# Optimization experiments

Hardware: AMD Instinct MI355X
Metric: run time of the kernel (lower is better)

The kernel has to match this reference:

```python
import jax, jax.numpy as jnp
import numpy as np

B, S, D_MODEL = 2, 2048, 2048
NUM_HEADS, NUM_KV_HEADS, HEAD_DIM = 16, 4, 128
MAX_SEQ = 2048
ROPE_WAVELENGTH = 10000.0


def apply_rope(x, positions, head_dim, max_wavelength):
    # x: [B, S, H, D], positions: [B, S]
    fraction = 2.0 * jnp.arange(0, head_dim // 2, dtype=jnp.float32) / head_dim
    timescale = max_wavelength ** fraction                      # [D/2]
    sinusoid = positions[..., None].astype(jnp.float32) / timescale  # [B,S,D/2]
    sin = jnp.sin(sinusoid)[:, :, None, :]                      # [B,S,1,D/2]
    cos = jnp.cos(sinusoid)[:, :, None, :]
    x1, x2 = jnp.split(x, 2, axis=-1)
    first = x1 * cos - x2 * sin
    second = x2 * cos + x1 * sin
    return jnp.concatenate([first, second], axis=-1).astype(x.dtype)


def setup_inputs() -> dict:
    key = jax.random.key(0)
    ks = jax.random.split(key, 5)
    inputs = jax.random.normal(ks[0], (B, S, D_MODEL), dtype=jnp.float32)
    seq_pos = jnp.broadcast_to(jnp.arange(S, dtype=jnp.int32)[None, :], (B, S))
    std = 0.01  # nnx.initializers.normal() default stddev
    wq = jax.random.normal(ks[1], (D_MODEL, NUM_HEADS, HEAD_DIM), dtype=jnp.float32) * std
    bq = jnp.zeros((NUM_HEADS, HEAD_DIM), dtype=jnp.float32)
    wkv = jax.random.normal(ks[2], (D_MODEL, NUM_KV_HEADS, 2 * HEAD_DIM), dtype=jnp.float32) * std
    bkv = jnp.zeros((NUM_KV_HEADS, 2 * HEAD_DIM), dtype=jnp.float32)
    wo = jax.random.normal(ks[3], (NUM_HEADS, HEAD_DIM, D_MODEL), dtype=jnp.float32) * std
    bo = jnp.zeros((D_MODEL,), dtype=jnp.float32)
    return {"inputs": inputs, "seq_pos": seq_pos, "wq": wq, "bq": bq,
            "wkv": wkv, "bkv": bkv, "wo": wo, "bo": bo}


def reference(inputs, seq_pos, wq, bq, wkv, bkv, wo, bo):
    dtype = inputs.dtype
    # Projections
    kv = jnp.einsum('bsd,dkh->bskh', inputs, wkv) + bkv          # [B,S,KV,2*HD]
    key, value = jnp.split(kv, 2, axis=-1)                       # [B,S,KV,HD] each
    query = jnp.einsum('bsd,dnh->bsnh', inputs, wq) + bq         # [B,S,H,HD]
    # RoPE
    query = apply_rope(query, seq_pos, HEAD_DIM, ROPE_WAVELENGTH)
    key = apply_rope(key, seq_pos, HEAD_DIM, ROPE_WAVELENGTH)
    # GQA: repeat KV heads
    rep = NUM_HEADS // NUM_KV_HEADS
    key_r = jnp.repeat(key, rep, axis=2)                          # [B,S,H,HD]
    value_r = jnp.repeat(value, rep, axis=2)
    # Attention (einsum_attention path)
    q = query / jnp.sqrt(jnp.asarray(HEAD_DIM, dtype=dtype))
    attn = jnp.einsum('bqhd,bkhd->bhqk', q, key_r)               # [B,H,S,S]
    # position_mask: seq_range <= time_steps -> causal
    seq_range = jnp.arange(MAX_SEQ, dtype=jnp.int32)
    mask = (seq_range[None, None, :] <= seq_pos[:, :, None])[:, None, :, :]  # [B,1,S,S]
    big_neg = jnp.finfo(dtype).min
    attn = jnp.where(mask, attn, big_neg)
    attn = jax.nn.softmax(attn, axis=-1).astype(dtype)
    x = jnp.einsum('bhqk,bkhd->bqhd', attn, value_r)             # [B,S,H,HD]
    out = jnp.einsum('bqhd,hdo->bqo', x, wo) + bo                # [B,S,D]
    return out
```

## Files before the change

### kernel.cpp

```cpp
#include <hip/hip_runtime.h>
#include <hip/hip_bf16.h>

#define DM    2048
#define SEQ   2048
#define NB    2
#define NH    16
#define NKVH  4
#define HD    128
#define NQKV  3072
#define MROWS 4096
#define KVB   64

using f32x4  = __attribute__((ext_vector_type(4))) float;
using short8 = __attribute__((ext_vector_type(8))) short;
using ushort8 = __attribute__((ext_vector_type(8))) unsigned short;

static __device__ __forceinline__ unsigned short f2bf(float f) {
  __hip_bfloat16 h = __float2bfloat16(f);
  return *reinterpret_cast<unsigned short*>(&h);
}
static __device__ __forceinline__ float bf2f(unsigned short u) {
  union { unsigned int i; float f; } v; v.i = ((unsigned int)u) << 16; return v.f;
}

typedef __attribute__((address_space(1))) const unsigned char as1_c;
typedef __attribute__((address_space(3))) unsigned char as3_c;
static __device__ __forceinline__ void gload_lds16(const void* g, void* l) {
  __builtin_amdgcn_global_load_lds((as1_c*)g, (as3_c*)l, 16, 0, 0);
}


__global__ void build_trig(float2* __restrict__ tbl) {
  int i = blockIdx.x * 256 + threadIdx.x;
  int p = i >> 6, d = i & 63;
  float inv_ts = powf(10000.0f, -(float)d * (1.0f / 64.0f));
  float ang = (float)p * inv_ts;
  float sn, cs;
  sincosf(ang, &sn, &cs);
  tbl[i] = make_float2(cs, sn);
}


__global__ void f32_to_bf16_vec(const float* __restrict__ src, unsigned short* __restrict__ dst, int n4) {
  int i = blockIdx.x * blockDim.x + threadIdx.x;
  if (i < n4) {
    float4 v = reinterpret_cast<const float4*>(src)[i];
    ushort4 o;
    o.x = f2bf(v.x); o.y = f2bf(v.y); o.z = f2bf(v.z); o.w = f2bf(v.w);
    reinterpret_cast<ushort4*>(dst)[i] = o;
  }
}

__global__ void transpose_all(const float* __restrict__ wq, const float* __restrict__ wkv,
                              const float* __restrict__ wo,
                              unsigned short* __restrict__ WqkvT, unsigned short* __restrict__ WoT) {
  int bx = blockIdx.x;
  const float* src; unsigned short* dst; int N;
  if (bx < 64)       { src = wq;  dst = WqkvT;                         N = 2048; }
  else if (bx < 96)  { src = wkv; dst = WqkvT + (size_t)2048 * DM;     N = 1024; bx -= 64; }
  else               { src = wo;  dst = WoT;                           N = 2048; bx -= 96; }
  __shared__ float t[32][33];
  int n0 = bx * 32, k0 = blockIdx.y * 32;
  int tx = threadIdx.x, ty = threadIdx.y;
  for (int j = 0; j < 4; j++)
    t[ty + j * 8][tx] = src[(size_t)(k0 + ty + j * 8) * N + n0 + tx];
  __syncthreads();
  for (int j = 0; j < 4; j++)
    dst[(size_t)(n0 + ty + j * 8) * DM + k0 + tx] = f2bf(t[tx][ty + j * 8]);
}

__global__ void bias_concat(const float* __restrict__ bq, const float* __restrict__ bkv, float* __restrict__ o) {
  int i = blockIdx.x * 256 + threadIdx.x;
  if (i < NQKV) o[i] = (i < DM) ? bq[i] : bkv[i - DM];
}


__global__ __launch_bounds__(256) void gemm_qkv(const unsigned short* __restrict__ A,
                                                const unsigned short* __restrict__ Bt,
                                                const float* __restrict__ bias,
                                                const int* __restrict__ seq_pos,
                                                const float2* __restrict__ tbl,
                                                unsigned short* __restrict__ Qo,
                                                unsigned short* __restrict__ Ko,
                                                unsigned short* __restrict__ Vo) {
  __shared__ __align__(16) unsigned short smem[128 * 136];
  unsigned short* la = smem;
  unsigned short* lb = smem + 128 * 64;
  const int K = DM;
  int tid = threadIdx.x, lane = tid & 63, w = tid >> 6;
  int wr = w >> 1, wc = w & 1, lg = lane >> 4, ln = lane & 15;
  int m0 = blockIdx.y * 128, n0 = blockIdx.x * 128;

  f32x4 acc[4][4];
  for (int mi = 0; mi < 4; mi++)
    for (int ni = 0; ni < 4; ni++) acc[mi][ni] = (f32x4){0, 0, 0, 0};

  int srow = lane >> 3;
  int scol = (lane & 7) * 8;
  const unsigned short* ga = A + (size_t)(m0 + w * 32 + srow) * K + scol;
  const unsigned short* gb = Bt + (size_t)(n0 + w * 32 + srow) * K + scol;
  unsigned short* lab = &la[(w * 32) * 64];
  unsigned short* lbb = &lb[(w * 32) * 64];

  for (int kt = 0; kt < K; kt += 64) {
#pragma unroll
    for (int i = 0; i < 4; i++) {
      gload_lds16(ga + (size_t)i * 8 * K + kt, lab + i * 8 * 64);
      gload_lds16(gb + (size_t)i * 8 * K + kt, lbb + i * 8 * 64);
    }
    __syncthreads();
#pragma unroll
    for (int kk = 0; kk < 64; kk += 32) {
      short8 af[4], bfr[4];
#pragma unroll
      for (int mi = 0; mi < 4; mi++)
        af[mi] = *reinterpret_cast<const short8*>(&la[(wr * 64 + mi * 16 + ln) * 64 + kk + lg * 8]);
#pragma unroll
      for (int ni = 0; ni < 4; ni++)
        bfr[ni] = *reinterpret_cast<const short8*>(&lb[(wc * 64 + ni * 16 + ln) * 64 + kk + lg * 8]);
#pragma unroll
      for (int mi = 0; mi < 4; mi++)
#pragma unroll
        for (int ni = 0; ni < 4; ni++)
          acc[mi][ni] = __builtin_amdgcn_mfma_f32_16x16x32_bf16(af[mi], bfr[ni], acc[mi][ni], 0, 0, 0);
    }
    __syncthreads();
  }

  __syncthreads();
#pragma unroll
  for (int mi = 0; mi < 4; mi++) {
    int row = wr * 64 + mi * 16 + lg * 4;
#pragma unroll
    for (int ni = 0; ni < 4; ni++) {
      int col = wc * 64 + ni * 16 + ln;
      float bv = bias[n0 + col];
#pragma unroll
      for (int r4 = 0; r4 < 4; r4++)
        smem[(row + r4) * 136 + col] = f2bf(acc[mi][ni][r4] + bv);
    }
  }
  __syncthreads();

  int nt = blockIdx.x;
  int b = m0 >> 11, s0 = m0 & (SEQ - 1);

  if (nt < 16 || !((nt - 16) & 1)) {
    float scale; unsigned short* dst;
    if (nt < 16) { scale = 0.08838834764831845f; dst = Qo + ((size_t)(b * NH + nt) * SEQ) * HD; }
    else         { scale = 1.0f; dst = Ko + ((size_t)(b * NKVH + ((nt - 16) >> 1)) * SEQ) * HD; }
    int sl = tid >> 1, dh = (tid & 1) * 32;
    int sg = s0 + sl;
    int pos = seq_pos[b * SEQ + sg];
    const float2* tp = tbl + pos * 64 + dh;
    ushort8 fb[4], sb2[4];
#pragma unroll
    for (int j = 0; j < 32; j++) {
      float x1 = bf2f(smem[sl * 136 + dh + j]);
      float x2 = bf2f(smem[sl * 136 + dh + j + 64]);
      float2 cs = tp[j];
      fb[j >> 3][j & 7]  = f2bf((x1 * cs.x - x2 * cs.y) * scale);
      sb2[j >> 3][j & 7] = f2bf((x2 * cs.x + x1 * cs.y) * scale);
    }
    unsigned short* dp = dst + (size_t)sg * HD + dh;
#pragma unroll
    for (int k = 0; k < 4; k++) {
      *reinterpret_cast<ushort8*>(dp + k * 8)      = fb[k];
      *reinterpret_cast<ushort8*>(dp + 64 + k * 8) = sb2[k];
    }
  } else {
    int kvh = (nt - 16) >> 1;
    int d = tid >> 1, sh = (tid & 1) * 64;
    ushort8 vb[8];
#pragma unroll
    for (int j = 0; j < 64; j++)
      vb[j >> 3][j & 7] = smem[(sh + j) * 136 + d];
    unsigned short* dp = Vo + ((size_t)(b * NKVH + kvh) * HD + d) * SEQ + s0 + sh;
#pragma unroll
    for (int k = 0; k < 8; k++)
      *reinterpret_cast<ushort8*>(dp + k * 8) = vb[k];
  }
}


__global__ __launch_bounds__(256) void gemm_bt(const unsigned short* __restrict__ A,
                                               const unsigned short* __restrict__ Bt,
                                               const float* __restrict__ bias,
                                               float* __restrict__ C, int M, int N, int K) {
  __shared__ __align__(16) unsigned short la[128 * 64];
  __shared__ __align__(16) unsigned short lb[128 * 64];
  int tid = threadIdx.x, lane = tid & 63, w = tid >> 6;
  int wr = w >> 1, wc = w & 1, lg = lane >> 4, ln = lane & 15;
  int m0 = blockIdx.y * 128, n0 = blockIdx.x * 128;

  f32x4 acc[4][4];
  for (int mi = 0; mi < 4; mi++)
    for (int ni = 0; ni < 4; ni++) acc[mi][ni] = (f32x4){0, 0, 0, 0};

  int srow = lane >> 3, scol = (lane & 7) * 8;
  const unsigned short* ga = A + (size_t)(m0 + w * 32 + srow) * K + scol;
  const unsigned short* gb = Bt + (size_t)(n0 + w * 32 + srow) * K + scol;
  unsigned short* lab = &la[(w * 32) * 64];
  unsigned short* lbb = &lb[(w * 32) * 64];

  for (int kt = 0; kt < K; kt += 64) {
#pragma unroll
    for (int i = 0; i < 4; i++) {
      gload_lds16(ga + (size_t)i * 8 * K + kt, lab + i * 8 * 64);
      gload_lds16(gb + (size_t)i * 8 * K + kt, lbb + i * 8 * 64);
    }
    __syncthreads();
#pragma unroll
    for (int kk = 0; kk < 64; kk += 32) {
      short8 af[4], bfr[4];
#pragma unroll
      for (int mi = 0; mi < 4; mi++)
        af[mi] = *reinterpret_cast<const short8*>(&la[(wr * 64 + mi * 16 + ln) * 64 + kk + lg * 8]);
#pragma unroll
      for (int ni = 0; ni < 4; ni++)
        bfr[ni] = *reinterpret_cast<const short8*>(&lb[(wc * 64 + ni * 16 + ln) * 64 + kk + lg * 8]);
#pragma unroll
      for (int mi = 0; mi < 4; mi++)
#pragma unroll
        for (int ni = 0; ni < 4; ni++)
          acc[mi][ni] = __builtin_amdgcn_mfma_f32_16x16x32_bf16(af[mi], bfr[ni], acc[mi][ni], 0, 0, 0);
    }
    __syncthreads();
  }
  for (int mi = 0; mi < 4; mi++) {
    int mrow = m0 + wr * 64 + mi * 16 + lg * 4;
    for (int ni = 0; ni < 4; ni++) {
      int n = n0 + wc * 64 + ni * 16 + ln;
      float bv = bias[n];
      for (int r4 = 0; r4 < 4; r4++)
        C[(size_t)(mrow + r4) * N + n] = acc[mi][ni][r4] + bv;
    }
  }
}


__global__ __launch_bounds__(256) void flash_attn(const unsigned short* __restrict__ Q,
                                                  const unsigned short* __restrict__ Kr,
                                                  const unsigned short* __restrict__ Vt,
                                                  const int* __restrict__ seq_pos,
                                                  unsigned short* __restrict__ X) {
  __shared__ __align__(16) unsigned short lds_k[64 * 128];
  __shared__ __align__(16) unsigned short lds_v[128 * 64];
  __shared__ __align__(16) unsigned short lds_p[4][16 * 64];
  int tid = threadIdx.x, lane = tid & 63, w = tid >> 6;
  int bh = blockIdx.y, b = bh >> 4, h = bh & 15, kvh = h >> 2;
  int lg = lane >> 4, ln = lane & 15;

  const unsigned short* kbase = Kr + ((size_t)(b * NKVH + kvh)) * SEQ * HD;
  const unsigned short* vbase = Vt + ((size_t)(b * NKVH + kvh)) * HD * SEQ;

  const unsigned short* gks[4]; unsigned short* lks[4];
  const unsigned short* gvs[4]; unsigned short* lvs[4];
#pragma unroll
  for (int i = 0; i < 4; i++) {
    int kr = w * 16 + i * 4 + (lane >> 4);
    int kc = (lane & 15) ^ (kr & 7);
    gks[i] = kbase + (size_t)kr * HD + kc * 8;
    lks[i] = lds_k + (w * 16 + i * 4) * 128;
    int vr = w * 32 + i * 8 + (lane >> 3);
    int vc = (lane & 7) ^ (vr & 7);
    gvs[i] = vbase + (size_t)vr * SEQ + vc * 8;
    lvs[i] = lds_v + (w * 32 + i * 8) * 64;
  }

  const short8 ones = {0x3F80, 0x3F80, 0x3F80, 0x3F80, 0x3F80, 0x3F80, 0x3F80, 0x3F80};

  for (int pass = 0; pass < 2; pass++) {
    int qtile = (pass == 0) ? (int)blockIdx.x : (SEQ / 64 - 1 - (int)blockIdx.x);
    int qblk = qtile * 64;
    int q0w = qblk + w * 16;

    int pmax = seq_pos[b * SEQ + qblk + lane];
    for (int o = 32; o; o >>= 1) { int t2 = __shfl_xor(pmax, o); pmax = pmax > t2 ? pmax : t2; }
    int ntiles = (pmax + KVB) >> 6;
    if (ntiles > SEQ / KVB) ntiles = SEQ / KVB;

    int pos_r[4];
    for (int r = 0; r < 4; r++) pos_r[r] = seq_pos[b * SEQ + q0w + lg * 4 + r];

    short8 qf[4];
    {
      const unsigned short* qp = Q + ((size_t)((b * NH + h) * SEQ + q0w + ln)) * HD;
      for (int c = 0; c < 4; c++) qf[c] = *reinterpret_cast<const short8*>(qp + c * 32 + lg * 8);
    }

    f32x4 acc[8];
    for (int dt = 0; dt < 8; dt++) acc[dt] = (f32x4){0, 0, 0, 0};
    f32x4 lacc = (f32x4){0, 0, 0, 0};
    float m_r[4] = {-1e30f, -1e30f, -1e30f, -1e30f};

    for (int t = 0; t < ntiles; t++) {
      int kv0 = t * KVB;
#pragma unroll
      for (int i = 0; i < 4; i++) {
        gload_lds16(gks[i] + (size_t)kv0 * HD, lks[i]);
        gload_lds16(gvs[i] + kv0, lvs[i]);
      }
      __syncthreads();

      f32x4 sa[4];
#pragma unroll
      for (int ct = 0; ct < 4; ct++) {
        sa[ct] = (f32x4){0, 0, 0, 0};
        int row = ct * 16 + ln;
        const char* kr0 = (const char*)lds_k + row * 256;
        int sw = (row & 7) << 4;
#pragma unroll
        for (int c = 0; c < 4; c++) {
          short8 kf = *reinterpret_cast<const short8*>(kr0 + ((c * 64 + lg * 16) ^ sw));
          sa[ct] = __builtin_amdgcn_mfma_f32_16x16x32_bf16(qf[c], kf, sa[ct], 0, 0, 0);
        }
      }

      float p[4][4], corr[4];
#pragma unroll
      for (int r = 0; r < 4; r++) {
        int kv = kv0 + ln;
        float v0 = (kv      <= pos_r[r]) ? sa[0][r] : -1e30f;
        float v1 = (kv + 16 <= pos_r[r]) ? sa[1][r] : -1e30f;
        float v2 = (kv + 32 <= pos_r[r]) ? sa[2][r] : -1e30f;
        float v3 = (kv + 48 <= pos_r[r]) ? sa[3][r] : -1e30f;
        float tmx = fmaxf(fmaxf(v0, v1), fmaxf(v2, v3));
        tmx = fmaxf(tmx, __shfl_xor(tmx, 1));
        tmx = fmaxf(tmx, __shfl_xor(tmx, 2));
        tmx = fmaxf(tmx, __shfl_xor(tmx, 4));
        tmx = fmaxf(tmx, __shfl_xor(tmx, 8));
        float nm = fmaxf(m_r[r], tmx);
        corr[r] = __expf(m_r[r] - nm);
        p[0][r] = __expf(v0 - nm); p[1][r] = __expf(v1 - nm);
        p[2][r] = __expf(v2 - nm); p[3][r] = __expf(v3 - nm);
        m_r[r] = nm;
      }

      {
        char* pw = (char*)lds_p[w];
#pragma unroll
        for (int r = 0; r < 4; r++) {
          int row = lg * 4 + r;
          int sw2 = (row & 7) << 4;
          char* pr = pw + row * 128;
#pragma unroll
          for (int ct = 0; ct < 4; ct++)
            *reinterpret_cast<unsigned short*>(pr + (((ct * 16 + ln) * 2) ^ sw2)) = f2bf(p[ct][r]);
        }
      }

#pragma unroll
      for (int dt = 0; dt < 8; dt++)
#pragma unroll
        for (int r = 0; r < 4; r++) acc[dt][r] *= corr[r];
#pragma unroll
      for (int r = 0; r < 4; r++) lacc[r] *= corr[r];

      asm volatile("s_waitcnt lgkmcnt(0)" ::: "memory");
      __builtin_amdgcn_sched_barrier(0);
      short8 pf[2];
      {
        const char* pr = (const char*)lds_p[w] + ln * 128;
        int sw2 = (ln & 7) << 4;
        pf[0] = *reinterpret_cast<const short8*>(pr + ((lg * 16) ^ sw2));
        pf[1] = *reinterpret_cast<const short8*>(pr + ((64 + lg * 16) ^ sw2));
      }

#pragma unroll
      for (int dt = 0; dt < 8; dt++) {
        int row = dt * 16 + ln;
        const char* vr0 = (const char*)lds_v + row * 128;
        int sw3 = (row & 7) << 4;
        short8 vf0 = *reinterpret_cast<const short8*>(vr0 + ((lg * 16) ^ sw3));
        short8 vf1 = *reinterpret_cast<const short8*>(vr0 + ((64 + lg * 16) ^ sw3));
        acc[dt] = __builtin_amdgcn_mfma_f32_16x16x32_bf16(pf[0], vf0, acc[dt], 0, 0, 0);
        acc[dt] = __builtin_amdgcn_mfma_f32_16x16x32_bf16(pf[1], vf1, acc[dt], 0, 0, 0);
      }
      lacc = __builtin_amdgcn_mfma_f32_16x16x32_bf16(pf[0], ones, lacc, 0, 0, 0);
      lacc = __builtin_amdgcn_mfma_f32_16x16x32_bf16(pf[1], ones, lacc, 0, 0, 0);
      __syncthreads();
    }

    for (int r = 0; r < 4; r++) {
      float inv = lacc[r] > 0.0f ? 1.0f / lacc[r] : 0.0f;
      int qrow = q0w + lg * 4 + r;
      unsigned short* xp = X + ((size_t)(b * SEQ + qrow)) * DM + h * HD;
      for (int dt = 0; dt < 8; dt++) xp[dt * 16 + ln] = f2bf(acc[dt][r] * inv);
    }
  }
}


extern "C" void kernel_launch(void* const* d_in, const int* in_sizes, int n_in,
                              void* d_out, int out_size, void* d_ws, size_t ws_size,
                              hipStream_t stream) {
  const float* inputs  = (const float*)d_in[0];
  const int*   seq_pos = (const int*)d_in[1];
  const float* wq  = (const float*)d_in[2];
  const float* bq  = (const float*)d_in[3];
  const float* wkv = (const float*)d_in[4];
  const float* bkv = (const float*)d_in[5];
  const float* wo  = (const float*)d_in[6];
  const float* bo  = (const float*)d_in[7];
  float* out = (float*)d_out;

  char* ws = (char*)d_ws;
  unsigned short* Abf     = (unsigned short*)(ws + 0);
  unsigned short* WqkvT   = (unsigned short*)(ws + 16777216);
  unsigned short* WoT     = (unsigned short*)(ws + 29360128);
  float*          biasqkv = (float*)(ws + 37748736);
  float2*         tbl     = (float2*)(ws + 37761024);
  unsigned short* Qr      = (unsigned short*)(ws + 38809600);
  unsigned short* Kr      = (unsigned short*)(ws + 55586816);
  unsigned short* Vt      = (unsigned short*)(ws + 59781120);
  unsigned short* Xb      = (unsigned short*)(ws + 63975424);

  build_trig<<<512, 256, 0, stream>>>(tbl);
  f32_to_bf16_vec<<<8192, 256, 0, stream>>>(inputs, Abf, (NB * SEQ * DM) / 4);
  transpose_all<<<dim3(160, 64), dim3(32, 8), 0, stream>>>(wq, wkv, wo, WqkvT, WoT);
  bias_concat<<<12, 256, 0, stream>>>(bq, bkv, biasqkv);

  gemm_qkv<<<dim3(NQKV / 128, MROWS / 128), 256, 0, stream>>>(
      Abf, WqkvT, biasqkv, seq_pos, tbl, Qr, Kr, Vt);

  flash_attn<<<dim3(SEQ / 128, NB * NH), 256, 0, stream>>>(Qr, Kr, Vt, seq_pos, Xb);

  gemm_bt<<<dim3(DM / 128, MROWS / 128), 256, 0, stream>>>(
      Xb, WoT, bo, out, MROWS, DM, DM);
}
```

Baseline: 362.3 us.

## Replace both projection GEMMs with pipelined 256x256 8-wave templated GEMM

Replaces the 128x128 single-buffered QKV and output GEMMs with one templated 256x256-tile, 512-thread kernel. It double-buffers LDS with interleaved async global-to-LDS loads between MFMA quarters and XOR-swizzles LDS to avoid bank conflicts. It also adds block-index swizzling for L2 locality and setprio around MFMA bursts. The QKV epilogue now applies RoPE, scaling and the V transpose straight from registers rather than through LDS. This trades a larger tile, more registers and a fixed 2-block occupancy for higher MFMA utilization and fewer blocks, which leaves fewer tiles per CU (192/128 blocks).

Result: faster. 314.6 us (-13.2%).

```diff
diff --git a/kernel.cpp b/kernel.cpp
--- a/kernel.cpp
+++ b/kernel.cpp
@@ -10,6 +10,7 @@
 #define NQKV  3072
 #define MROWS 4096
 #define KVB   64
+#define QSC   0.08838834764831845f
 
 using f32x4  = __attribute__((ext_vector_type(4))) float;
 using short8 = __attribute__((ext_vector_type(8))) short;
@@ -75,165 +76,176 @@
 }
 
 
-__global__ __launch_bounds__(256) void gemm_qkv(const unsigned short* __restrict__ A,
-                                                const unsigned short* __restrict__ Bt,
-                                                const float* __restrict__ bias,
-                                                const int* __restrict__ seq_pos,
-                                                const float2* __restrict__ tbl,
-                                                unsigned short* __restrict__ Qo,
-                                                unsigned short* __restrict__ Ko,
-                                                unsigned short* __restrict__ Vo) {
-  __shared__ __align__(16) unsigned short smem[128 * 136];
-  unsigned short* la = smem;
-  unsigned short* lb = smem + 128 * 64;
-  const int K = DM;
+#define STA(buf, kt, q) gload_lds16(gA + (size_t)((q) * 32) * K + (kt), LW + (buf) * 65536 + ((q) * 32 + rowA) * 128)
+#define STB(buf, kt, h) gload_lds16(gB + (size_t)((h) * 64) * K + (kt), LW + (buf) * 65536 + 32768 + ((h) * 64 + rowB) * 128)
+
+#define RDB(buf) \
+  _Pragma("unroll") for (int ni = 0; ni < 4; ++ni) { \
+    int row_ = (EPI == 1) ? (wc * 16 + ni * 64 + ln) : (wc * 64 + ni * 16 + ln); \
+    const char* p_ = (const char*)LW + (buf) * 65536 + 32768 + row_ * 128; \
+    bfr[ni][0] = *(const short8*)(p_ + coff0); \
+    bfr[ni][1] = *(const short8*)(p_ + coff1); }
+
+#define RDA(buf, q) \
+  _Pragma("unroll") for (int m2 = 0; m2 < 2; ++m2) { \
+    int row_ = wr * 128 + ((q) * 2 + m2) * 16 + ln; \
+    const char* p_ = (const char*)LW + (buf) * 65536 + row_ * 128; \
+    af[m2][0] = *(const short8*)(p_ + coff0); \
+    af[m2][1] = *(const short8*)(p_ + coff1); }
+
+#define MFQ(q) \
+  _Pragma("unroll") for (int m2 = 0; m2 < 2; ++m2) \
+  _Pragma("unroll") for (int ni = 0; ni < 4; ++ni) { \
+    acc[(q) * 2 + m2][ni] = __builtin_amdgcn_mfma_f32_16x16x32_bf16(af[m2][0], bfr[ni][0], acc[(q) * 2 + m2][ni], 0, 0, 0); \
+    acc[(q) * 2 + m2][ni] = __builtin_amdgcn_mfma_f32_16x16x32_bf16(af[m2][1], bfr[ni][1], acc[(q) * 2 + m2][ni], 0, 0, 0); }
+
+#define SYNC_IN() do { __builtin_amdgcn_sched_barrier(0); __builtin_amdgcn_s_barrier(); \
+  asm volatile("s_waitcnt lgkmcnt(0)" ::: "memory"); __builtin_amdgcn_sched_barrier(0); \
+  __builtin_amdgcn_s_setprio(1); } while (0)
+#define SYNC_OUT() do { __builtin_amdgcn_s_setprio(0); __builtin_amdgcn_sched_barrier(0); \
+  __builtin_amdgcn_s_barrier(); } while (0)
+#define SYNC_OUT_VM() do { __builtin_amdgcn_s_setprio(0); \
+  asm volatile("s_waitcnt vmcnt(6)" ::: "memory"); __builtin_amdgcn_sched_barrier(0); \
+  __builtin_amdgcn_s_barrier(); } while (0)
+
+template <int EPI>
+__global__ __launch_bounds__(512, 2) void gemm8(
+    const unsigned short* __restrict__ A, const unsigned short* __restrict__ Bt,
+    const float* __restrict__ bias, const int* __restrict__ seq_pos,
+    const float2* __restrict__ tbl,
+    unsigned short* __restrict__ Qo, unsigned short* __restrict__ Ko,
+    unsigned short* __restrict__ Vo, float* __restrict__ Cout,
+    int nbx, int N, int K) {
+  __shared__ __align__(16) unsigned short lds[2 * 2 * 16384];
   int tid = threadIdx.x, lane = tid & 63, w = tid >> 6;
-  int wr = w >> 1, wc = w & 1, lg = lane >> 4, ln = lane & 15;
-  int m0 = blockIdx.y * 128, n0 = blockIdx.x * 128;
-
-  f32x4 acc[4][4];
-  for (int mi = 0; mi < 4; mi++)
-    for (int ni = 0; ni < 4; ni++) acc[mi][ni] = (f32x4){0, 0, 0, 0};
-
-  int srow = lane >> 3;
-  int scol = (lane & 7) * 8;
-  const unsigned short* ga = A + (size_t)(m0 + w * 32 + srow) * K + scol;
-  const unsigned short* gb = Bt + (size_t)(n0 + w * 32 + srow) * K + scol;
-  unsigned short* lab = &la[(w * 32) * 64];
-  unsigned short* lbb = &lb[(w * 32) * 64];
-
-  for (int kt = 0; kt < K; kt += 64) {
-#pragma unroll
-    for (int i = 0; i < 4; i++) {
-      gload_lds16(ga + (size_t)i * 8 * K + kt, lab + i * 8 * 64);
-      gload_lds16(gb + (size_t)i * 8 * K + kt, lbb + i * 8 * 64);
-    }
-    __syncthreads();
-#pragma unroll
-    for (int kk = 0; kk < 64; kk += 32) {
-      short8 af[4], bfr[4];
-#pragma unroll
-      for (int mi = 0; mi < 4; mi++)
-        af[mi] = *reinterpret_cast<const short8*>(&la[(wr * 64 + mi * 16 + ln) * 64 + kk + lg * 8]);
-#pragma unroll
-      for (int ni = 0; ni < 4; ni++)
-        bfr[ni] = *reinterpret_cast<const short8*>(&lb[(wc * 64 + ni * 16 + ln) * 64 + kk + lg * 8]);
-#pragma unroll
-      for (int mi = 0; mi < 4; mi++)
-#pragma unroll
-        for (int ni = 0; ni < 4; ni++)
-          acc[mi][ni] = __builtin_amdgcn_mfma_f32_16x16x32_bf16(af[mi], bfr[ni], acc[mi][ni], 0, 0, 0);
-    }
-    __syncthreads();
+  int wr = w >> 2, wc = w & 3;
+  int lg = lane >> 4, ln = lane & 15;
+
+  int bid = blockIdx.x;
+  int cpx = gridDim.x >> 3;
+  int swz = (bid & 7) * cpx + (bid >> 3);
+  int by = swz / nbx, bx = swz - by * nbx;
+  int m0 = by * 256, n0 = bx * 256;
+
+  int soff = ((lane & 7) ^ (lane >> 3)) << 3;
+  const unsigned short* gA = A + (size_t)(m0 + ((w & 3) << 3) + ((w >> 2) << 7) + (lane >> 3)) * K + soff;
+  const unsigned short* gB = Bt + (size_t)(n0 + (w << 3) + (lane >> 3)) * K + soff;
+  char* LW = (char*)lds;
+  int rowA = ((w & 3) << 3) + ((w >> 2) << 7);
+  int rowB = (w << 3);
+  int coff0 = ((lg)     ^ (ln & 7)) << 4;
+  int coff1 = ((lg + 4) ^ (ln & 7)) << 4;
+
+  f32x4 acc[8][4];
+#pragma unroll
+  for (int mi = 0; mi < 8; ++mi)
+#pragma unroll
+    for (int ni = 0; ni < 4; ++ni) acc[mi][ni] = (f32x4){0, 0, 0, 0};
+
+  short8 bfr[4][2], af[2][2];
+
+  STB(0, 0, 0); STB(0, 0, 1); STB(0, 0, 2); STB(0, 0, 3);
+  STA(0, 0, 0); STA(0, 0, 1); STA(0, 0, 2); STA(0, 0, 3);
+  STB(1, 64, 0); STB(1, 64, 1); STB(1, 64, 2); STB(1, 64, 3);
+  STA(1, 64, 0); STA(1, 64, 1);
+  asm volatile("s_waitcnt vmcnt(6)" ::: "memory");
+  __builtin_amdgcn_sched_barrier(0);
+  __builtin_amdgcn_s_barrier();
+
+  for (int it = 0; it < (K >> 7); ++it) {
+    int kt1  = it * 128 + 64;
+    int ktn0 = (it * 128 + 128) & (K - 1);
+    int ktn1 = (it * 128 + 192) & (K - 1);
+    RDB(0); RDA(0, 0);
+    STA(1, kt1, 2); STA(1, kt1, 3);
+    SYNC_IN(); MFQ(0); SYNC_OUT();
+    RDA(0, 1);
+    STB(0, ktn0, 0); STB(0, ktn0, 1);
+    SYNC_IN(); MFQ(1); SYNC_OUT();
+    RDA(0, 2);
+    STB(0, ktn0, 2); STB(0, ktn0, 3);
+    SYNC_IN(); MFQ(2); SYNC_OUT();
+    RDA(0, 3);
+    STA(0, ktn0, 0); STA(0, ktn0, 1);
+    SYNC_IN(); MFQ(3); SYNC_OUT_VM();
+    RDB(1); RDA(1, 0);
+    STA(0, ktn0, 2); STA(0, ktn0, 3);
+    SYNC_IN(); MFQ(0); SYNC_OUT();
+    RDA(1, 1);
+    STB(1, ktn1, 0); STB(1, ktn1, 1);
+    SYNC_IN(); MFQ(1); SYNC_OUT();
+    RDA(1, 2);
+    STB(1, ktn1, 2); STB(1, ktn1, 3);
+    SYNC_IN(); MFQ(2); SYNC_OUT();
+    RDA(1, 3);
+    STA(1, ktn1, 0); STA(1, ktn1, 1);
+    SYNC_IN(); MFQ(3); SYNC_OUT_VM();
   }
-
-  __syncthreads();
-#pragma unroll
-  for (int mi = 0; mi < 4; mi++) {
-    int row = wr * 64 + mi * 16 + lg * 4;
-#pragma unroll
-    for (int ni = 0; ni < 4; ni++) {
-      int col = wc * 64 + ni * 16 + ln;
-      float bv = bias[n0 + col];
-#pragma unroll
-      for (int r4 = 0; r4 < 4; r4++)
-        smem[(row + r4) * 136 + col] = f2bf(acc[mi][ni][r4] + bv);
-    }
-  }
-  __syncthreads();
-
-  int nt = blockIdx.x;
-  int b = m0 >> 11, s0 = m0 & (SEQ - 1);
-
-  if (nt < 16 || !((nt - 16) & 1)) {
-    float scale; unsigned short* dst;
-    if (nt < 16) { scale = 0.08838834764831845f; dst = Qo + ((size_t)(b * NH + nt) * SEQ) * HD; }
-    else         { scale = 1.0f; dst = Ko + ((size_t)(b * NKVH + ((nt - 16) >> 1)) * SEQ) * HD; }
-    int sl = tid >> 1, dh = (tid & 1) * 32;
-    int sg = s0 + sl;
-    int pos = seq_pos[b * SEQ + sg];
-    const float2* tp = tbl + pos * 64 + dh;
-    ushort8 fb[4], sb2[4];
-#pragma unroll
-    for (int j = 0; j < 32; j++) {
-      float x1 = bf2f(smem[sl * 136 + dh + j]);
-      float x2 = bf2f(smem[sl * 136 + dh + j + 64]);
-      float2 cs = tp[j];
-      fb[j >> 3][j & 7]  = f2bf((x1 * cs.x - x2 * cs.y) * scale);
-      sb2[j >> 3][j & 7] = f2bf((x2 * cs.x + x1 * cs.y) * scale);
-    }
-    unsigned short* dp = dst + (size_t)sg * HD + dh;
-#pragma unroll
-    for (int k = 0; k < 4; k++) {
-      *reinterpret_cast<ushort8*>(dp + k * 8)      = fb[k];
-      *reinterpret_cast<ushort8*>(dp + 64 + k * 8) = sb2[k];
+  asm volatile("s_waitcnt vmcnt(0)" ::: "memory");
+
+  if constexpr (EPI == 0) {
+#pragma unroll
+    for (int mi = 0; mi < 8; ++mi) {
+      int row = m0 + wr * 128 + mi * 16 + lg * 4;
+#pragma unroll
+      for (int ni = 0; ni < 4; ++ni) {
+        int col = n0 + wc * 64 + ni * 16 + ln;
+        float bv = bias[col];
+#pragma unroll
+        for (int r = 0; r < 4; ++r)
+          Cout[(size_t)(row + r) * N + col] = acc[mi][ni][r] + bv;
+      }
     }
   } else {
-    int kvh = (nt - 16) >> 1;
-    int d = tid >> 1, sh = (tid & 1) * 64;
-    ushort8 vb[8];
-#pragma unroll
-    for (int j = 0; j < 64; j++)
-      vb[j >> 3][j & 7] = smem[(sh + j) * 136 + d];
-    unsigned short* dp = Vo + ((size_t)(b * NKVH + kvh) * HD + d) * SEQ + s0 + sh;
-#pragma unroll
-    for (int k = 0; k < 8; k++)
-      *reinterpret_cast<ushort8*>(dp + k * 8) = vb[k];
-  }
-}
-
-
-__global__ __launch_bounds__(256) void gemm_bt(const unsigned short* __restrict__ A,
-                                               const unsigned short* __restrict__ Bt,
-                                               const float* __restrict__ bias,
-                                               float* __restrict__ C, int M, int N, int K) {
-  __shared__ __align__(16) unsigned short la[128 * 64];
-  __shared__ __align__(16) unsigned short lb[128 * 64];
-  int tid = threadIdx.x, lane = tid & 63, w = tid >> 6;
-  int wr = w >> 1, wc = w & 1, lg = lane >> 4, ln = lane & 15;
-  int m0 = blockIdx.y * 128, n0 = blockIdx.x * 128;
-
-  f32x4 acc[4][4];
-  for (int mi = 0; mi < 4; mi++)
-    for (int ni = 0; ni < 4; ni++) acc[mi][ni] = (f32x4){0, 0, 0, 0};
-
-  int srow = lane >> 3, scol = (lane & 7) * 8;
-  const unsigned short* ga = A + (size_t)(m0 + w * 32 + srow) * K + scol;
-  const unsigned short* gb = Bt + (size_t)(n0 + w * 32 + srow) * K + scol;
-  unsigned short* lab = &la[(w * 32) * 64];
-  unsigned short* lbb = &lb[(w * 32) * 64];
-
-  for (int kt = 0; kt < K; kt += 64) {
-#pragma unroll
-    for (int i = 0; i < 4; i++) {
-      gload_lds16(ga + (size_t)i * 8 * K + kt, lab + i * 8 * 64);
-      gload_lds16(gb + (size_t)i * 8 * K + kt, lbb + i * 8 * 64);
-    }
-    __syncthreads();
-#pragma unroll
-    for (int kk = 0; kk < 64; kk += 32) {
-      short8 af[4], bfr[4];
-#pragma unroll
-      for (int mi = 0; mi < 4; mi++)
-        af[mi] = *reinterpret_cast<const short8*>(&la[(wr * 64 + mi * 16 + ln) * 64 + kk + lg * 8]);
-#pragma unroll
-      for (int ni = 0; ni < 4; ni++)
-        bfr[ni] = *reinterpret_cast<const short8*>(&lb[(wc * 64 + ni * 16 + ln) * 64 + kk + lg * 8]);
-#pragma unroll
-      for (int mi = 0; mi < 4; mi++)
-#pragma unroll
-        for (int ni = 0; ni < 4; ni++)
-          acc[mi][ni] = __builtin_amdgcn_mfma_f32_16x16x32_bf16(af[mi], bfr[ni], acc[mi][ni], 0, 0, 0);
-    }
-    __syncthreads();
-  }
-  for (int mi = 0; mi < 4; mi++) {
-    int mrow = m0 + wr * 64 + mi * 16 + lg * 4;
-    for (int ni = 0; ni < 4; ni++) {
-      int n = n0 + wc * 64 + ni * 16 + ln;
-      float bv = bias[n];
-      for (int r4 = 0; r4 < 4; r4++)
-        C[(size_t)(mrow + r4) * N + n] = acc[mi][ni][r4] + bv;
+    int d = wc * 16 + ln;
+    float bv0 = bias[n0 + d],      bv1 = bias[n0 + d + 64];
+    float bv2 = bias[n0 + d + 128], bv3 = bias[n0 + d + 192];
+    int bI = m0 >> 11, s0 = m0 & (SEQ - 1);
+    int nt = n0 >> 8;
+    if (nt < 8) {
+      unsigned short* qp0 = Qo + (size_t)(bI * NH + nt * 2) * SEQ * HD;
+      unsigned short* qp1 = qp0 + (size_t)SEQ * HD;
+#pragma unroll
+      for (int mi = 0; mi < 8; ++mi) {
+        int sl = wr * 128 + mi * 16 + lg * 4;
+#pragma unroll
+        for (int r = 0; r < 4; ++r) {
+          int s = s0 + sl + r;
+          int pos = seq_pos[bI * SEQ + s];
+          float2 cs = tbl[pos * 64 + d];
+          float x1 = acc[mi][0][r] + bv0, x2 = acc[mi][1][r] + bv1;
+          float y1 = acc[mi][2][r] + bv2, y2 = acc[mi][3][r] + bv3;
+          unsigned short* q0 = qp0 + (size_t)s * HD;
+          q0[d]      = f2bf((x1 * cs.x - x2 * cs.y) * QSC);
+          q0[d + 64] = f2bf((x2 * cs.x + x1 * cs.y) * QSC);
+          unsigned short* q1 = qp1 + (size_t)s * HD;
+          q1[d]      = f2bf((y1 * cs.x - y2 * cs.y) * QSC);
+          q1[d + 64] = f2bf((y2 * cs.x + y1 * cs.y) * QSC);
+        }
+      }
+    } else {
+      int kvh = nt - 8;
+      unsigned short* kp = Ko + (size_t)(bI * NKVH + kvh) * SEQ * HD;
+      unsigned short* vp = Vo + (size_t)(bI * NKVH + kvh) * HD * SEQ;
+#pragma unroll
+      for (int mi = 0; mi < 8; ++mi) {
+        int sl = wr * 128 + mi * 16 + lg * 4;
+        ushort4 v0q, v1q;
+#pragma unroll
+        for (int r = 0; r < 4; ++r) {
+          int s = s0 + sl + r;
+          int pos = seq_pos[bI * SEQ + s];
+          float2 cs = tbl[pos * 64 + d];
+          float x1 = acc[mi][0][r] + bv0, x2 = acc[mi][1][r] + bv1;
+          unsigned short* krow = kp + (size_t)s * HD;
+          krow[d]      = f2bf(x1 * cs.x - x2 * cs.y);
+          krow[d + 64] = f2bf(x2 * cs.x + x1 * cs.y);
+          ((unsigned short*)&v0q)[r] = f2bf(acc[mi][2][r] + bv2);
+          ((unsigned short*)&v1q)[r] = f2bf(acc[mi][3][r] + bv3);
+        }
+        *(ushort4*)(vp + (size_t)d * SEQ + s0 + sl)        = v0q;
+        *(ushort4*)(vp + (size_t)(d + 64) * SEQ + s0 + sl) = v1q;
+      }
     }
   }
 }
@@ -421,11 +433,11 @@
   transpose_all<<<dim3(160, 64), dim3(32, 8), 0, stream>>>(wq, wkv, wo, WqkvT, WoT);
   bias_concat<<<12, 256, 0, stream>>>(bq, bkv, biasqkv);
 
-  gemm_qkv<<<dim3(NQKV / 128, MROWS / 128), 256, 0, stream>>>(
-      Abf, WqkvT, biasqkv, seq_pos, tbl, Qr, Kr, Vt);
+  gemm8<1><<<(MROWS / 256) * (NQKV / 256), 512, 0, stream>>>(
+      Abf, WqkvT, biasqkv, seq_pos, tbl, Qr, Kr, Vt, nullptr, NQKV / 256, NQKV, DM);
 
   flash_attn<<<dim3(SEQ / 128, NB * NH), 256, 0, stream>>>(Qr, Kr, Vt, seq_pos, Xb);
 
-  gemm_bt<<<dim3(DM / 128, MROWS / 128), 256, 0, stream>>>(
-      Xb, WoT, bo, out, MROWS, DM, DM);
-}
+  gemm8<0><<<(MROWS / 256) * (DM / 256), 512, 0, stream>>>(
+      Xb, WoT, bo, nullptr, nullptr, nullptr, nullptr, nullptr, out, DM / 256, DM, DM);
+}
```
